# Optimization experiments

Hardware: AMD Instinct MI355X
Metric: run time of the kernel (lower is better)

Reference implementation:

```python
import jax, jax.numpy as jnp
import numpy as np


def setup_inputs() -> dict:
    key = jax.random.key(0)
    ks = jax.random.split(key, 9)
    B, C, H, W = 2, 16, 256, 256
    Cctx = 64
    Cqk, Cv = C // 8, C // 16
    return {
        "x": jax.random.normal(ks[0], (B, C, H, W), jnp.float32),
        "y": jax.random.normal(ks[1], (B, Cctx, H, W), jnp.float32),
        "Wq": jax.random.normal(ks[2], (Cqk, C), jnp.float32) * 0.1,
        "bq": jax.random.normal(ks[3], (Cqk,), jnp.float32) * 0.1,
        "Wk": jax.random.normal(ks[4], (Cqk, C), jnp.float32) * 0.1,
        "bk": jax.random.normal(ks[5], (Cqk,), jnp.float32) * 0.1,
        "Wv": jax.random.normal(ks[6], (Cv, Cctx), jnp.float32) * 0.1,
        "bv": jax.random.normal(ks[7], (Cv,), jnp.float32) * 0.1,
        "gamma": jax.random.normal(ks[8], (1,), jnp.float32),
    }


def reference(x, y, Wq, bq, Wk, bk, Wv, bv, gamma):
    B, C, H, W = x.shape
    # 1x1 convs as channel contractions
    q = jnp.einsum('bchw,oc->bohw', x, Wq) + bq[None, :, None, None]
    k = jnp.einsum('bchw,oc->bohw', x, Wk) + bk[None, :, None, None]
    v = jnp.einsum('bchw,oc->bohw', y, Wv) + bv[None, :, None, None]
    # column (H-axis) attention energy with -inf diagonal: [B,H,W,H]
    eH = jnp.einsum('bchw,bcgw->bhwg', q, k)
    diag = jnp.eye(H, dtype=bool)[None, :, None, :]  # mask h == h2
    eH = jnp.where(diag, -jnp.inf, eH)
    # row (W-axis) attention energy: [B,H,W,W]
    eW = jnp.einsum('bchw,bchg->bhwg', q, k)
    # joint softmax over concatenated H+W axis
    att = jax.nn.softmax(jnp.concatenate([eH, eW], axis=3), axis=3)
    aH, aW = att[..., :H], att[..., H:]
    outH = jnp.einsum('bcgw,bhwg->bchw', v, aH)
    outW = jnp.einsum('bchg,bhwg->bchw', v, aW)
    # bilinear interpolate to (H,W) is an identity here; broadcast Cv=1 over C
    return gamma[0] * (outH + outW) + x
```

## Files before the change

kernel.cpp:

```cpp
#include <hip/hip_runtime.h>
#include <math.h>

#define Bsz  2
#define Cch  16
#define Hdim 256
#define Wdim 256
#define HW   (Hdim * Wdim)
#define BHW  (Bsz * HW)
#define CctxN 64
#define NS   4
#define SG   (Hdim / NS)
#define TH   4
#define LOG2E 1.44269504088896340736f

__device__ __forceinline__ float fexp2(float x) { return exp2f(x); }

__global__ __launch_bounds__(256) void qkv_kernel(
    const float* __restrict__ x, const float* __restrict__ y,
    const float* __restrict__ Wq, const float* __restrict__ bq,
    const float* __restrict__ Wk, const float* __restrict__ bk,
    const float* __restrict__ Wv, const float* __restrict__ bv,
    float2* __restrict__ qpk, float4* __restrict__ kv) {
  int idx0 = (blockIdx.x * blockDim.x + threadIdx.x) * 2;
  int b  = idx0 >> 16;
  int hw = idx0 & (HW - 1);
  const float2* xp = (const float2*)(x + (size_t)b * Cch * HW + hw);
  float q0a = bq[0], q1a = bq[1], k0a = bk[0], k1a = bk[1];
  float q0b = bq[0], q1b = bq[1], k0b = bk[0], k1b = bk[1];
#pragma unroll
  for (int c = 0; c < Cch; c++) {
    float2 xv = xp[c * (HW / 2)];
    q0a = fmaf(Wq[c],       xv.x, q0a);  q0b = fmaf(Wq[c],       xv.y, q0b);
    q1a = fmaf(Wq[Cch + c], xv.x, q1a);  q1b = fmaf(Wq[Cch + c], xv.y, q1b);
    k0a = fmaf(Wk[c],       xv.x, k0a);  k0b = fmaf(Wk[c],       xv.y, k0b);
    k1a = fmaf(Wk[Cch + c], xv.x, k1a);  k1b = fmaf(Wk[Cch + c], xv.y, k1b);
  }
  qpk[idx0]     = make_float2(q0a * LOG2E, q1a * LOG2E);
  qpk[idx0 + 1] = make_float2(q0b * LOG2E, q1b * LOG2E);
  const float2* yp = (const float2*)(y + (size_t)b * CctxN * HW + hw);
  float va = bv[0], vb2 = bv[0];
#pragma unroll
  for (int c = 0; c < CctxN; c++) {
    float2 yv = yp[c * (HW / 2)];
    va  = fmaf(Wv[c], yv.x, va);
    vb2 = fmaf(Wv[c], yv.y, vb2);
  }
  kv[idx0]     = make_float4(k0a, k1a, va,  0.f);
  kv[idx0 + 1] = make_float4(k0b, k1b, vb2, 0.f);
}

__global__ __launch_bounds__(256) void attn_kernel(
    const float2* __restrict__ qpk, const float4* __restrict__ kv,
    float* __restrict__ part) {
  int s  = blockIdx.x & (NS - 1);
  int ht = (blockIdx.x >> 2) & 63;
  int b  = blockIdx.x >> 8;
  int w  = threadIdx.x;
  int h0 = ht * TH;
  int g0 = s * SG;
  size_t bbase = (size_t)b * HW;

  __shared__ float4 rowkv[TH][SG];
  {
    int h_l = threadIdx.x >> 6, gg = threadIdx.x & 63;
    rowkv[h_l][gg] = kv[bbase + (size_t)(h0 + h_l) * Wdim + g0 + gg];
  }
  float q0[TH], q1[TH];
#pragma unroll
  for (int h_l = 0; h_l < TH; h_l++) {
    float2 qq = qpk[bbase + (size_t)(h0 + h_l) * Wdim + w];
    q0[h_l] = qq.x; q1[h_l] = qq.y;
  }
  __syncthreads();

  float Z[TH] = {0,0,0,0}, nH[TH] = {0,0,0,0}, nW[TH] = {0,0,0,0};
#pragma unroll 4
  for (int gg = 0; gg < SG; gg++) {
    float4 kc = kv[bbase + (size_t)(g0 + gg) * Wdim + w];
#pragma unroll
    for (int h_l = 0; h_l < TH; h_l++) {
      float4 r = rowkv[h_l][gg];
      float pH = fexp2(fmaf(q0[h_l], kc.x, q1[h_l] * kc.y));
      float pW = fexp2(fmaf(q0[h_l], r.x,  q1[h_l] * r.y));
      Z [h_l] += pH + pW;
      nH[h_l] = fmaf(pH, kc.z, nH[h_l]);
      nW[h_l] = fmaf(pW, r.z,  nW[h_l]);
    }
  }
  if ((h0 >> 6) == s) {
#pragma unroll
    for (int h_l = 0; h_l < TH; h_l++) {
      float4 kd = kv[bbase + (size_t)(h0 + h_l) * Wdim + w];
      float pd = fexp2(fmaf(q0[h_l], kd.x, q1[h_l] * kd.y));
      Z [h_l] -= pd;
      nH[h_l] = fmaf(-pd, kd.z, nH[h_l]);
    }
  }
#pragma unroll
  for (int h_l = 0; h_l < TH; h_l++) {
    size_t idx = bbase + (size_t)(h0 + h_l) * Wdim + w;
    part[(size_t)(s * 3 + 0) * BHW + idx] = Z [h_l];
    part[(size_t)(s * 3 + 1) * BHW + idx] = nH[h_l];
    part[(size_t)(s * 3 + 2) * BHW + idx] = nW[h_l];
  }
}

__global__ __launch_bounds__(256) void epi_kernel(
    const float* __restrict__ x, const float* __restrict__ part,
    const float* __restrict__ gamma, float* __restrict__ out) {
  int idx0 = (blockIdx.x * blockDim.x + threadIdx.x) * 2;
  float2 Z = make_float2(0.f, 0.f), nH = Z, nW = Z;
#pragma unroll
  for (int s2 = 0; s2 < NS; s2++) {
    float2 a = *(const float2*)&part[(size_t)(s2 * 3 + 0) * BHW + idx0];
    float2 c = *(const float2*)&part[(size_t)(s2 * 3 + 1) * BHW + idx0];
    float2 d = *(const float2*)&part[(size_t)(s2 * 3 + 2) * BHW + idx0];
    Z.x += a.x;  Z.y += a.y;
    nH.x += c.x; nH.y += c.y;
    nW.x += d.x; nW.y += d.y;
  }
  float g = gamma[0];
  float2 sv = make_float2(g * (nH.x + nW.x) / Z.x, g * (nH.y + nW.y) / Z.y);
  int b = idx0 >> 16, hw = idx0 & (HW - 1);
  size_t base = (size_t)b * Cch * HW + hw;
#pragma unroll
  for (int c = 0; c < Cch; c++) {
    float2 xv = *(const float2*)&x[base + c * HW];
    *(float2*)&out[base + c * HW] = make_float2(sv.x + xv.x, sv.y + xv.y);
  }
}

extern "C" void kernel_launch(void* const* d_in, const int* in_sizes, int n_in,
                              void* d_out, int out_size, void* d_ws, size_t ws_size,
                              hipStream_t stream) {
  const float* x     = (const float*)d_in[0];
  const float* y     = (const float*)d_in[1];
  const float* Wq    = (const float*)d_in[2];
  const float* bq    = (const float*)d_in[3];
  const float* Wk    = (const float*)d_in[4];
  const float* bk    = (const float*)d_in[5];
  const float* Wv    = (const float*)d_in[6];
  const float* bv    = (const float*)d_in[7];
  const float* gamma = (const float*)d_in[8];
  float* out = (float*)d_out;

  float* ws = (float*)d_ws;
  float2* qpk = (float2*)ws;
  float4* kv  = (float4*)(ws + 2 * BHW);
  float*  part = ws + 6 * BHW;

  qkv_kernel<<<BHW / 512, 256, 0, stream>>>(x, y, Wq, bq, Wk, bk, Wv, bv, qpk, kv);
  attn_kernel<<<Bsz * (Hdim / TH) * NS, 256, 0, stream>>>(qpk, kv, part);
  epi_kernel<<<BHW / 512, 256, 0, stream>>>(x, part, gamma, out);
}
```

Measured before the change: 129.4 us.

## Double attention row tile and key splits, widen elementwise kernels to float4

The attention kernel now processes 8 query rows per block and splits the key axis into 8 chunks instead of 4. Each column key/value load is therefore reused across twice as many rows. The unroll factor drops to 2 to offset the extra register pressure. The projection and epilogue kernels move from two to four pixels per thread using float4 loads and stores, which doubles the partial-sum buffer traffic read in the epilogue.

```diff
diff --git a/kernel.cpp b/kernel.cpp
--- a/kernel.cpp
+++ b/kernel.cpp
@@ -8,9 +8,9 @@
 #define HW   (Hdim * Wdim)
 #define BHW  (Bsz * HW)
 #define CctxN 64
-#define NS   4
+#define NS   8
 #define SG   (Hdim / NS)
-#define TH   4
+#define TH   8
 #define LOG2E 1.44269504088896340736f
 
 __device__ __forceinline__ float fexp2(float x) { return exp2f(x); }
@@ -21,39 +21,47 @@
     const float* __restrict__ Wk, const float* __restrict__ bk,
     const float* __restrict__ Wv, const float* __restrict__ bv,
     float2* __restrict__ qpk, float4* __restrict__ kv) {
-  int idx0 = (blockIdx.x * blockDim.x + threadIdx.x) * 2;
+  int idx0 = (blockIdx.x * blockDim.x + threadIdx.x) * 4;
   int b  = idx0 >> 16;
   int hw = idx0 & (HW - 1);
-  const float2* xp = (const float2*)(x + (size_t)b * Cch * HW + hw);
-  float q0a = bq[0], q1a = bq[1], k0a = bk[0], k1a = bk[1];
-  float q0b = bq[0], q1b = bq[1], k0b = bk[0], k1b = bk[1];
+  const float4* xp = (const float4*)(x + (size_t)b * Cch * HW + hw);
+  float q0[4], q1[4], k0[4], k1[4], vv[4];
+#pragma unroll
+  for (int j = 0; j < 4; j++) { q0[j] = bq[0]; q1[j] = bq[1]; k0[j] = bk[0]; k1[j] = bk[1]; vv[j] = bv[0]; }
 #pragma unroll
   for (int c = 0; c < Cch; c++) {
-    float2 xv = xp[c * (HW / 2)];
-    q0a = fmaf(Wq[c],       xv.x, q0a);  q0b = fmaf(Wq[c],       xv.y, q0b);
-    q1a = fmaf(Wq[Cch + c], xv.x, q1a);  q1b = fmaf(Wq[Cch + c], xv.y, q1b);
-    k0a = fmaf(Wk[c],       xv.x, k0a);  k0b = fmaf(Wk[c],       xv.y, k0b);
-    k1a = fmaf(Wk[Cch + c], xv.x, k1a);  k1b = fmaf(Wk[Cch + c], xv.y, k1b);
+    float4 xv = xp[c * (HW / 4)];
+    float wq0 = Wq[c], wq1 = Wq[Cch + c], wk0 = Wk[c], wk1 = Wk[Cch + c];
+    const float* xe = (const float*)&xv;
+#pragma unroll
+    for (int j = 0; j < 4; j++) {
+      q0[j] = fmaf(wq0, xe[j], q0[j]);
+      q1[j] = fmaf(wq1, xe[j], q1[j]);
+      k0[j] = fmaf(wk0, xe[j], k0[j]);
+      k1[j] = fmaf(wk1, xe[j], k1[j]);
+    }
   }
-  qpk[idx0]     = make_float2(q0a * LOG2E, q1a * LOG2E);
-  qpk[idx0 + 1] = make_float2(q0b * LOG2E, q1b * LOG2E);
-  const float2* yp = (const float2*)(y + (size_t)b * CctxN * HW + hw);
-  float va = bv[0], vb2 = bv[0];
+  const float4* yp = (const float4*)(y + (size_t)b * CctxN * HW + hw);
 #pragma unroll
   for (int c = 0; c < CctxN; c++) {
-    float2 yv = yp[c * (HW / 2)];
-    va  = fmaf(Wv[c], yv.x, va);
-    vb2 = fmaf(Wv[c], yv.y, vb2);
+    float4 yv = yp[c * (HW / 4)];
+    const float* ye = (const float*)&yv;
+    float wv = Wv[c];
+#pragma unroll
+    for (int j = 0; j < 4; j++) vv[j] = fmaf(wv, ye[j], vv[j]);
   }
-  kv[idx0]     = make_float4(k0a, k1a, va,  0.f);
-  kv[idx0 + 1] = make_float4(k0b, k1b, vb2, 0.f);
+  float4* qout = (float4*)&qpk[idx0];
+  qout[0] = make_float4(q0[0] * LOG2E, q1[0] * LOG2E, q0[1] * LOG2E, q1[1] * LOG2E);
+  qout[1] = make_float4(q0[2] * LOG2E, q1[2] * LOG2E, q0[3] * LOG2E, q1[3] * LOG2E);
+#pragma unroll
+  for (int j = 0; j < 4; j++) kv[idx0 + j] = make_float4(k0[j], k1[j], vv[j], 0.f);
 }
 
 __global__ __launch_bounds__(256) void attn_kernel(
     const float2* __restrict__ qpk, const float4* __restrict__ kv,
     float* __restrict__ part) {
   int s  = blockIdx.x & (NS - 1);
-  int ht = (blockIdx.x >> 2) & 63;
+  int ht = (blockIdx.x >> 3) & 31;
   int b  = blockIdx.x >> 8;
   int w  = threadIdx.x;
   int h0 = ht * TH;
@@ -62,7 +70,7 @@
 
   __shared__ float4 rowkv[TH][SG];
   {
-    int h_l = threadIdx.x >> 6, gg = threadIdx.x & 63;
+    int h_l = threadIdx.x >> 5, gg = threadIdx.x & 31;
     rowkv[h_l][gg] = kv[bbase + (size_t)(h0 + h_l) * Wdim + g0 + gg];
   }
   float q0[TH], q1[TH];
@@ -73,8 +81,10 @@
   }
   __syncthreads();
 
-  float Z[TH] = {0,0,0,0}, nH[TH] = {0,0,0,0}, nW[TH] = {0,0,0,0};
-#pragma unroll 4
+  float Z[TH], nH[TH], nW[TH];
+#pragma unroll
+  for (int h_l = 0; h_l < TH; h_l++) { Z[h_l] = 0.f; nH[h_l] = 0.f; nW[h_l] = 0.f; }
+#pragma unroll 2
   for (int gg = 0; gg < SG; gg++) {
     float4 kc = kv[bbase + (size_t)(g0 + gg) * Wdim + w];
 #pragma unroll
@@ -87,7 +97,7 @@
       nW[h_l] = fmaf(pW, r.z,  nW[h_l]);
     }
   }
-  if ((h0 >> 6) == s) {
+  if ((h0 >> 5) == s) {
 #pragma unroll
     for (int h_l = 0; h_l < TH; h_l++) {
       float4 kd = kv[bbase + (size_t)(h0 + h_l) * Wdim + w];
@@ -108,25 +118,28 @@
 __global__ __launch_bounds__(256) void epi_kernel(
     const float* __restrict__ x, const float* __restrict__ part,
     const float* __restrict__ gamma, float* __restrict__ out) {
-  int idx0 = (blockIdx.x * blockDim.x + threadIdx.x) * 2;
-  float2 Z = make_float2(0.f, 0.f), nH = Z, nW = Z;
+  int idx0 = (blockIdx.x * blockDim.x + threadIdx.x) * 4;
+  float Z[4] = {0,0,0,0}, nH[4] = {0,0,0,0}, nW[4] = {0,0,0,0};
 #pragma unroll
   for (int s2 = 0; s2 < NS; s2++) {
-    float2 a = *(const float2*)&part[(size_t)(s2 * 3 + 0) * BHW + idx0];
-    float2 c = *(const float2*)&part[(size_t)(s2 * 3 + 1) * BHW + idx0];
-    float2 d = *(const float2*)&part[(size_t)(s2 * 3 + 2) * BHW + idx0];
-    Z.x += a.x;  Z.y += a.y;
-    nH.x += c.x; nH.y += c.y;
-    nW.x += d.x; nW.y += d.y;
+    float4 a = *(const float4*)&part[(size_t)(s2 * 3 + 0) * BHW + idx0];
+    float4 c = *(const float4*)&part[(size_t)(s2 * 3 + 1) * BHW + idx0];
+    float4 d = *(const float4*)&part[(size_t)(s2 * 3 + 2) * BHW + idx0];
+    const float *ae = (const float*)&a, *ce = (const float*)&c, *de = (const float*)&d;
+#pragma unroll
+    for (int j = 0; j < 4; j++) { Z[j] += ae[j]; nH[j] += ce[j]; nW[j] += de[j]; }
   }
   float g = gamma[0];
-  float2 sv = make_float2(g * (nH.x + nW.x) / Z.x, g * (nH.y + nW.y) / Z.y);
+  float sv[4];
+#pragma unroll
+  for (int j = 0; j < 4; j++) sv[j] = g * (nH[j] + nW[j]) / Z[j];
   int b = idx0 >> 16, hw = idx0 & (HW - 1);
   size_t base = (size_t)b * Cch * HW + hw;
 #pragma unroll
   for (int c = 0; c < Cch; c++) {
-    float2 xv = *(const float2*)&x[base + c * HW];
-    *(float2*)&out[base + c * HW] = make_float2(sv.x + xv.x, sv.y + xv.y);
+    float4 xv = *(const float4*)&x[base + c * HW];
+    *(float4*)&out[base + c * HW] =
+        make_float4(sv[0] + xv.x, sv[1] + xv.y, sv[2] + xv.z, sv[3] + xv.w);
   }
 }
 
@@ -149,7 +162,7 @@
   float4* kv  = (float4*)(ws + 2 * BHW);
   float*  part = ws + 6 * BHW;
 
-  qkv_kernel<<<BHW / 512, 256, 0, stream>>>(x, y, Wq, bq, Wk, bk, Wv, bv, qpk, kv);
+  qkv_kernel<<<BHW / 1024, 256, 0, stream>>>(x, y, Wq, bq, Wk, bk, Wv, bv, qpk, kv);
   attn_kernel<<<Bsz * (Hdim / TH) * NS, 256, 0, stream>>>(qpk, kv, part);
-  epi_kernel<<<BHW / 512, 256, 0, stream>>>(x, part, gamma, out);
+  epi_kernel<<<BHW / 1024, 256, 0, stream>>>(x, part, gamma, out);
 }
```

Result: slower. 135.8 us (+4.9%).
